# Optimization experiments

Measured on AMD Instinct MI355X. Metric: run time of the kernel, lower is better.

## Reference

```python
import jax, jax.numpy as jnp
import numpy as np

B, C, OUT, H, W, M1, M2, HID = 4, 64, 64, 256, 256, 32, 32, 64
COORD = C + 1  # MLP input: channels + 1 coordinate


def _lin(key, fan_in, fan_out):
    lim = 1.0 / np.sqrt(fan_in)
    kw, kb = jax.random.split(key)
    Wm = jax.random.uniform(kw, (fan_in, fan_out), minval=-lim, maxval=lim, dtype=jnp.float32)
    b = jax.random.uniform(kb, (fan_out,), minval=-lim, maxval=lim, dtype=jnp.float32)
    return Wm, b


def setup_inputs() -> dict:
    key = jax.random.key(0)
    ks = jax.random.split(key, 12)
    x = jax.random.normal(ks[0], (B, C, H, W), dtype=jnp.float32)
    # basis_w MLP: (C+1) -> HID -> HID -> 2*M2
    wW0, wb0 = _lin(ks[1], COORD, HID)
    wW1, wb1 = _lin(ks[2], HID, HID)
    wW2, wb2 = _lin(ks[3], HID, 2 * M2)
    # basis_h MLP: (C+1) -> HID -> HID -> 2*M1
    hW0, hb0 = _lin(ks[4], COORD, HID)
    hW1, hb1 = _lin(ks[5], HID, HID)
    hW2, hb2 = _lin(ks[6], HID, 2 * M1)
    std = (1.0 / (C + OUT)) ** 0.5
    Wf_re = std * jax.random.normal(ks[7], (C, OUT, M1, M2), dtype=jnp.float32)
    Wf_im = std * jax.random.normal(ks[8], (C, OUT, M1, M2), dtype=jnp.float32)
    mixer_w, mixer_b = _lin(ks[9], OUT, OUT)
    mixer_w = mixer_w.T  # (out, in) conv1x1 layout
    sc_w, sc_b = _lin(ks[10], C, OUT)
    sc_w = sc_w.T
    return {
        "x": x,
        "wW0": wW0, "wb0": wb0, "wW1": wW1, "wb1": wb1, "wW2": wW2, "wb2": wb2,
        "hW0": hW0, "hb0": hb0, "hW1": hW1, "hb1": hb1, "hW2": hW2, "hb2": hb2,
        "Wf_re": Wf_re, "Wf_im": Wf_im,
        "mixer_w": mixer_w, "mixer_b": mixer_b,
        "sc_w": sc_w, "sc_b": sc_b,
    }


def _gelu(v):
    return jax.nn.gelu(v, approximate=False)  # torch GELU is exact erf


def _cmlp(x, W0, b0, W1, b1, W2, b2, m):
    h = _gelu(x @ W0 + b0)
    h = _gelu(h @ W1 + b1)
    o = h @ W2 + b2
    return jax.lax.complex(o[..., :m], o[..., m:])


def reference(x, wW0, wb0, wW1, wb1, wW2, wb2,
              hW0, hb0, hW1, hb1, hW2, hb2,
              Wf_re, Wf_im, mixer_w, mixer_b, sc_w, sc_b):
    Bb, Cc, Hh, Ww = x.shape
    # --- W-direction basis: input is (values, w-coord) per pixel ---
    wc = jnp.linspace(-1.0, 1.0, Ww, dtype=jnp.float32)
    w_in = jnp.concatenate(
        [jnp.transpose(x, (0, 2, 3, 1)),
         jnp.broadcast_to(wc[None, None, :, None], (Bb, Hh, Ww, 1))], axis=-1)
    wb = _cmlp(w_in, wW0, wb0, wW1, wb1, wW2, wb2, M2)  # (B,H,W,m2) complex
    xc = x.astype(jnp.complex64)
    # separable transform along W: contract W against runtime basis
    tfw = jnp.einsum('bchw,bhwm->bchm', xc, wb)  # (B,C,H,m2)
    # --- H-direction basis: input is real part of W-transform + h-coord ---
    hcv = jnp.linspace(-1.0, 1.0, Hh, dtype=jnp.float32)
    h_in = jnp.concatenate(
        [jnp.transpose(tfw.real, (0, 3, 2, 1)),
         jnp.broadcast_to(hcv[None, None, :, None], (Bb, M2, Hh, 1))], axis=-1)
    hb = _cmlp(h_in, hW0, hb0, hW1, hb1, hW2, hb2, M1)  # (B,m2,H,m1) complex
    tfhw = jnp.einsum('bchm,bmhk->bckm', tfw, hb)  # (B,C,m1,m2)
    Wf = jax.lax.complex(Wf_re, Wf_im)  # (C_in, C_out, m1, m2)
    proc = jnp.einsum('bixy,oixy->boxy', tfhw, Wf)  # (B,out,m1,m2)
    # inverse transforms with conjugate-transposed bases
    rec = jnp.einsum('bokm,bmhk->bohm', proc, jnp.conj(hb))  # (B,out,H,m2)
    spatial = jnp.einsum('bohm,bhwm->bohw', rec, jnp.conj(wb)).real / (Hh * Ww)
    y = jnp.einsum('bchw,oc->bohw', spatial, mixer_w) + mixer_b[None, :, None, None]
    y = _gelu(y)
    y = y + jnp.einsum('bchw,oc->bohw', x, sc_w) + sc_b[None, :, None, None]
    return _gelu(y)
```

## Files before the change

kernel.cpp:

```cpp
#include <hip/hip_runtime.h>
#include <math.h>


typedef __attribute__((ext_vector_type(8))) short bf16x8;
typedef __attribute__((ext_vector_type(4))) float f32x4;

__device__ __forceinline__ float gelu_f(float v) {
    const float u = v * 0.70710678118654752440f;
    const float xa = fabsf(u);
    const float t = __builtin_amdgcn_rcpf(fmaf(0.3275911f, xa, 1.0f));
    float p = fmaf(1.061405429f, t, -1.453152027f);
    p = fmaf(p, t, 1.421413741f);
    p = fmaf(p, t, -0.284496736f);
    p = fmaf(p, t, 0.254829592f);
    p *= t;
    const float e = __expf(-xa * xa);
    float erfv = fmaf(-p, e, 1.0f);
    erfv = (u < 0.0f) ? -erfv : erfv;
    return 0.5f * v * (1.0f + erfv);
}

__device__ __forceinline__ unsigned short f2b(float f) {
    union { float f; unsigned int u; } v; v.f = f;
    unsigned int u = v.u + 0x7FFFu + ((v.u >> 16) & 1u);
    return (unsigned short)(u >> 16);
}
__device__ __forceinline__ float b2f(unsigned short b) {
    union { unsigned int u; float f; } v; v.u = ((unsigned int)b) << 16;
    return v.f;
}

__device__ __forceinline__ ushort4 butterfly_xT(const float4 v, int q) {
    const float bx = __shfl_xor(v.x, 1);
    const float by = __shfl_xor(v.y, 1);
    const float bz = __shfl_xor(v.z, 1);
    const float bw = __shfl_xor(v.w, 1);
    float4 s1;
    s1.x = ((q & 1) == 0) ? v.x : by;
    s1.y = ((q & 1) == 0) ? bx  : v.y;
    s1.z = ((q & 1) == 0) ? v.z : bw;
    s1.w = ((q & 1) == 0) ? bz  : v.w;
    const float cx = __shfl_xor(s1.x, 2);
    const float cy = __shfl_xor(s1.y, 2);
    const float cz = __shfl_xor(s1.z, 2);
    const float cw = __shfl_xor(s1.w, 2);
    float4 s2;
    s2.x = ((q & 2) == 0) ? s1.x : cz;
    s2.y = ((q & 2) == 0) ? s1.y : cw;
    s2.z = ((q & 2) == 0) ? cx   : s1.z;
    s2.w = ((q & 2) == 0) ? cy   : s1.w;
    ushort4 u;
    u.x = f2b(s2.x); u.y = f2b(s2.y); u.z = f2b(s2.z); u.w = f2b(s2.w);
    return u;
}

__device__ __forceinline__ void stage_xT(const float* __restrict__ x,
    unsigned short* __restrict__ sA, int b, int h, int w0, int t, int LD)
{
    const int lane = t & 63, wv = t >> 6;
    const int q = lane & 3, wg = lane >> 2;
#pragma unroll
    for (int r = 0; r < 4; ++r) {
        const int cb = (r * 4 + wv) * 4;
        const float4 v = *(const float4*)&x[((size_t)(b * 64 + cb + q) * 256 + h) * 256 + w0 + wg * 4];
        const ushort4 u = butterfly_xT(v, q);
        *(ushort4*)&sA[(wg * 4 + q) * LD + cb] = u;
    }
}

__global__ void k_prep(const float* __restrict__ wW0, const float* __restrict__ wW1,
                       const float* __restrict__ wW2,
                       const float* __restrict__ hW0, const float* __restrict__ hW1,
                       const float* __restrict__ hW2,
                       unsigned short* __restrict__ wT0, unsigned short* __restrict__ wT1,
                       unsigned short* __restrict__ wT2,
                       unsigned short* __restrict__ hT0, unsigned short* __restrict__ hT1,
                       unsigned short* __restrict__ hT2)
{
    const int t = threadIdx.x;
    for (int idx = t; idx < 64 * 96; idx += 256) {
        const int o = idx / 96, k = idx % 96;
        wT0[idx] = (k < 65) ? f2b(wW0[k * 64 + o]) : (unsigned short)0;
        hT0[idx] = (k < 65) ? f2b(hW0[k * 64 + o]) : (unsigned short)0;
    }
    for (int idx = t; idx < 4096; idx += 256) {
        const int o = idx >> 6, k = idx & 63;
        wT1[idx] = f2b(wW1[k * 64 + o]);
        wT2[idx] = f2b(wW2[k * 64 + o]);
        hT1[idx] = f2b(hW1[k * 64 + o]);
        hT2[idx] = f2b(hW2[k * 64 + o]);
    }
}

__global__ __launch_bounds__(256) void k_psum(const float* __restrict__ src,
                                              float* __restrict__ dst,
                                              int nparts, int part_stride)
{
    const int i = (blockIdx.x * 256 + threadIdx.x) * 4;
    float4 acc = *(const float4*)&src[i];
    for (int p = 1; p < nparts; ++p) {
        const float4 v = *(const float4*)&src[(size_t)p * part_stride + i];
        acc.x += v.x; acc.y += v.y; acc.z += v.z; acc.w += v.w;
    }
    *(float4*)&dst[i] = acc;
}

__global__ __launch_bounds__(256) void k_psum_procT(const float* __restrict__ src,
                                                    float* __restrict__ dst)
{
    const int idx = blockIdx.x * 256 + threadIdx.x;
    const int o = idx & 63, k = (idx >> 6) & 31, m = (idx >> 11) & 31, b = idx >> 16;
    const size_t in = (size_t)(b * 64 + o) * 1024 + k * 32 + m;
    const float re = src[in] + src[524288 + in];
    const float im = src[262144 + in] + src[524288 + 262144 + in];
    dst[idx] = re;
    dst[262144 + idx] = im;
}

template<bool GELU, int NKC>
__device__ __forceinline__ void mfma_layer_r(
    const bf16x8* __restrict__ wf,
    const unsigned short* __restrict__ sAct,
    unsigned short* __restrict__ dst,
    const float4 bv, int arow, int g, int wv)
{
    const int crow = 16 * wv + g * 4;
    const int sx7 = arow & 7, sx3 = arow & 3;
    const f32x4 zero = {0.f, 0.f, 0.f, 0.f};
    f32x4 acc[4] = {zero, zero, zero, zero};
#pragma unroll
    for (int kc = 0; kc < NKC; ++kc) {
        const int chraw = kc * 4 + g;
        const int ch = (chraw < 8) ? (chraw ^ sx7) : (8 + ((chraw - 8) ^ sx3));
#pragma unroll
        for (int nt = 0; nt < 4; ++nt) {
            const bf16x8 b = *(const bf16x8*)&sAct[(nt * 16 + arow) * 96 + ch * 8];
            acc[nt] = __builtin_amdgcn_mfma_f32_16x16x32_bf16(wf[kc], b, acc[nt], 0, 0, 0);
        }
    }
    const int chw = (crow >> 3) ^ sx7;
#pragma unroll
    for (int nt = 0; nt < 4; ++nt) {
        const int px = nt * 16 + arow;
        float v0 = acc[nt][0] + bv.x;
        float v1 = acc[nt][1] + bv.y;
        float v2 = acc[nt][2] + bv.z;
        float v3 = acc[nt][3] + bv.w;
        if (GELU) { v0 = gelu_f(v0); v1 = gelu_f(v1); v2 = gelu_f(v2); v3 = gelu_f(v3); }
        ushort4 u;
        u.x = f2b(v0); u.y = f2b(v1); u.z = f2b(v2); u.w = f2b(v3);
        *(ushort4*)&dst[px * 96 + chw * 8 + (crow & 7)] = u;
    }
}

__device__ __forceinline__ float4 load_xtile(const float* __restrict__ x,
    int b, int h, int w0, int lane, int wv, int r)
{
    const int q = lane & 3, wg = lane >> 2;
    const int cb = 16 * r + 4 * wv;
    return *(const float4*)&x[((size_t)(b * 64 + cb + q) * 256 + h) * 256 + w0 + wg * 4];
}

__global__ __launch_bounds__(256) void k_wbtfw(
    const float* __restrict__ x,
    const unsigned short* __restrict__ wT0, const float* __restrict__ b0,
    const unsigned short* __restrict__ wT1, const float* __restrict__ b1,
    const unsigned short* __restrict__ wT2, const float* __restrict__ b2,
    unsigned short* __restrict__ wb_bf, unsigned short* __restrict__ tfwM)
{
    __shared__ __align__(16) unsigned short smem[20480];
    unsigned short* sA   = smem;
    unsigned short* sB   = smem + 6144;
    unsigned short* sXt  = smem + 12288;
    unsigned short* sWBt = smem + 16384;

    const int bh = blockIdx.x;
    const int b = bh >> 8, h = bh & 255;
    const int t = threadIdx.x;
    const int lane = t & 63, wv = t >> 6;
    const int arow = lane & 15, g = lane >> 4;
    const int crow = 16 * wv + g * 4;
    const int sx7 = arow & 7;
    const f32x4 zero = {0.f, 0.f, 0.f, 0.f};

    const int wrow = 16 * wv + arow;
    bf16x8 w0f[3], w1f[2], w2f[2];
#pragma unroll
    for (int kc = 0; kc < 3; ++kc)
        w0f[kc] = *(const bf16x8*)&wT0[wrow * 96 + (kc * 4 + g) * 8];
#pragma unroll
    for (int kc = 0; kc < 2; ++kc) {
        w1f[kc] = *(const bf16x8*)&wT1[wrow * 64 + (kc * 4 + g) * 8];
        w2f[kc] = *(const bf16x8*)&wT2[wrow * 64 + (kc * 4 + g) * 8];
    }
    const float4 bv0 = *(const float4*)&b0[crow];
    const float4 bv1 = *(const float4*)&b1[crow];
    const float4 bv2 = *(const float4*)&b2[crow];

    f32x4 atf[4] = {zero, zero, zero, zero};

    float4 xv[4];
#pragma unroll
    for (int r = 0; r < 4; ++r) xv[r] = load_xtile(x, b, h, 0, lane, wv, r);

    for (int wq = 0; wq < 4; ++wq) {
        const int w0 = wq * 64;
        __syncthreads();
        {
            const int q = lane & 3, wg = lane >> 2;
#pragma unroll
            for (int r = 0; r < 4; ++r) {
                const int cb = 16 * r + 4 * wv;
                const int c = cb + q;
                const float4 v = xv[r];
                ushort4 ux;
                ux.x = f2b(v.x); ux.y = f2b(v.y); ux.z = f2b(v.z); ux.w = f2b(v.w);
                const int chx = (wg >> 1) ^ (c & 7);
                *(ushort4*)&sXt[c * 64 + chx * 8 + 4 * (wg & 1)] = ux;
                const ushort4 u = butterfly_xT(v, q);
                const int row = wg * 4 + q;
                const int cha = (cb >> 3) ^ (row & 7);
                *(ushort4*)&sA[row * 96 + cha * 8 + (cb & 7)] = u;
            }
        }
        if (t < 64) {
            const uint4 z = {0, 0, 0, 0};
#pragma unroll
            for (int j = 0; j < 4; ++j)
                *(uint4*)&sA[t * 96 + (8 + (j ^ (t & 3))) * 8] = z;
            sA[t * 96 + (8 + (t & 3)) * 8] = f2b((float)(w0 + t) * (2.0f / 255.0f) - 1.0f);
        }
        float4 xn[4];
        if (wq < 3) {
            const int w0n = (wq + 1) * 64;
#pragma unroll
            for (int r = 0; r < 4; ++r) xn[r] = load_xtile(x, b, h, w0n, lane, wv, r);
        }
        __syncthreads();
        mfma_layer_r<true, 3>(w0f, sA, sB, bv0, arow, g, wv);
        __syncthreads();
        mfma_layer_r<true, 2>(w1f, sB, sA, bv1, arow, g, wv);
        __syncthreads();
        {
            f32x4 acc[4] = {zero, zero, zero, zero};
#pragma unroll
            for (int kc = 0; kc < 2; ++kc) {
                const int ch = (kc * 4 + g) ^ sx7;
#pragma unroll
                for (int nt = 0; nt < 4; ++nt) {
                    const bf16x8 bb = *(const bf16x8*)&sA[(nt * 16 + arow) * 96 + ch * 8];
                    acc[nt] = __builtin_amdgcn_mfma_f32_16x16x32_bf16(w2f[kc], bb, acc[nt], 0, 0, 0);
                }
            }
            const int chw = (crow >> 3) ^ sx7;
#pragma unroll
            for (int nt = 0; nt < 4; ++nt) {
                const int px = nt * 16 + arow;
                ushort4 u;
                u.x = f2b(acc[nt][0] + bv2.x);
                u.y = f2b(acc[nt][1] + bv2.y);
                u.z = f2b(acc[nt][2] + bv2.z);
                u.w = f2b(acc[nt][3] + bv2.w);
                *(ushort4*)&sB[px * 96 + chw * 8 + (crow & 7)] = u;
                const int ph = px >> 3, pl = px & 7;
                sWBt[(crow + 0) * 64 + ((ph ^ ((crow + 0) & 7)) << 3) + pl] = u.x;
                sWBt[(crow + 1) * 64 + ((ph ^ ((crow + 1) & 7)) << 3) + pl] = u.y;
                sWBt[(crow + 2) * 64 + ((ph ^ ((crow + 2) & 7)) << 3) + pl] = u.z;
                sWBt[(crow + 3) * 64 + ((ph ^ ((crow + 3) & 7)) << 3) + pl] = u.w;
            }
        }
        __syncthreads();
        const size_t pixbase = (size_t)(b * 256 + h) * 256 + w0;
#pragma unroll
        for (int r = 0; r < 2; ++r) {
            const int idx = r * 256 + t;
            const int px = idx >> 3, f = idx & 7;
            *(uint4*)&wb_bf[(pixbase + px) * 64 + f * 8] =
                *(const uint4*)&sB[px * 96 + ((f ^ (px & 7)) << 3)];
        }
#pragma unroll
        for (int kc = 0; kc < 2; ++kc) {
            const int ch = (kc * 4 + g) ^ sx7;
            const bf16x8 a = *(const bf16x8*)&sWBt[(16 * wv + arow) * 64 + ch * 8];
#pragma unroll
            for (int nt = 0; nt < 4; ++nt) {
                const bf16x8 bb = *(const bf16x8*)&sXt[(nt * 16 + arow) * 64 + ch * 8];
                atf[nt] = __builtin_amdgcn_mfma_f32_16x16x32_bf16(a, bb, atf[nt], 0, 0, 0);
            }
        }
        if (wq < 3) {
#pragma unroll
            for (int r = 0; r < 4; ++r) xv[r] = xn[r];
        }
    }

    __syncthreads();
    float* sF = (float*)smem;
#pragma unroll
    for (int nt = 0; nt < 4; ++nt) {
        const int c = nt * 16 + arow;
#pragma unroll
        for (int j = 0; j < 4; ++j)
            sF[(crow + j) * 68 + c] = atf[nt][j];
    }
    __syncthreads();
#pragma unroll
    for (int r = 0; r < 4; ++r) {
        const int idx = r * 256 + t;
        const int m = idx >> 5, gg = idx & 31;
        ushort4 u;
        u.x = f2b(sF[m * 68 + gg * 2]);
        u.y = f2b(sF[(m + 32) * 68 + gg * 2]);
        u.z = f2b(sF[m * 68 + gg * 2 + 1]);
        u.w = f2b(sF[(m + 32) * 68 + gg * 2 + 1]);
        *(ushort4*)&tfwM[((size_t)(b * 32 + m) * 256 + h) * 128 + gg * 4] = u;
    }
}

__global__ __launch_bounds__(256) void k_hbtfhw(
    const unsigned short* __restrict__ tfwM,
    const unsigned short* __restrict__ hT0, const float* __restrict__ b0,
    const unsigned short* __restrict__ hT1, const float* __restrict__ b1,
    const unsigned short* __restrict__ hT2, const float* __restrict__ b2,
    unsigned short* __restrict__ hb_bf, float* __restrict__ tfhw_p)
{
    __shared__ __align__(16) unsigned short smem[14336];
    unsigned short* sB = smem;
    unsigned short* sA = smem + 6144;
    float* slab = (float*)(smem + 6144);

    const int blk = blockIdx.x;
    const int bm = blk >> 2, hq = blk & 3;
    const int b = bm >> 5, m = bm & 31;
    const int h0 = hq * 64;
    const int t = threadIdx.x;
    const int lane = t & 63, wv = t >> 6;
    const int arow = lane & 15, g = lane >> 4;
    const int crow = 16 * wv + g * 4;

    const int wrow = 16 * wv + arow;
    bf16x8 h0f[3], h1f[2], h2f[2];
#pragma unroll
    for (int kc = 0; kc < 3; ++kc)
        h0f[kc] = *(const bf16x8*)&hT0[wrow * 96 + (kc * 4 + g) * 8];
#pragma unroll
    for (int kc = 0; kc < 2; ++kc) {
        h1f[kc] = *(const bf16x8*)&hT1[wrow * 64 + (kc * 4 + g) * 8];
        h2f[kc] = *(const bf16x8*)&hT2[wrow * 64 + (kc * 4 + g) * 8];
    }
    const float4 bv0 = *(const float4*)&b0[crow];
    const float4 bv1 = *(const float4*)&b1[crow];
    const float4 bv2 = *(const float4*)&b2[crow];

#pragma unroll
    for (int r = 0; r < 4; ++r) {
        const int idx = r * 256 + t;
        const int p = idx >> 4, f = idx & 15;
        const uint4 raw = *(const uint4*)&tfwM[((size_t)(bm * 256 + h0 + p)) * 128 + f * 8];
        const unsigned short* s = (const unsigned short*)&raw;
        ushort4 u;
        u.x = s[0]; u.y = s[2]; u.z = s[4]; u.w = s[6];
        const int ch = (f >> 1) ^ (p & 7);
        *(ushort4*)&sA[p * 96 + ch * 8 + 4 * (f & 1)] = u;
    }
    if (t < 64) {
        const uint4 z = {0, 0, 0, 0};
#pragma unroll
        for (int j = 0; j < 4; ++j)
            *(uint4*)&sA[t * 96 + (8 + (j ^ (t & 3))) * 8] = z;
        sA[t * 96 + (8 + (t & 3)) * 8] = f2b((float)(h0 + t) * (2.0f / 255.0f) - 1.0f);
    }
    __syncthreads();
    mfma_layer_r<true, 3>(h0f, sA, sB, bv0, arow, g, wv);
    __syncthreads();
    mfma_layer_r<true, 2>(h1f, sB, sA, bv1, arow, g, wv);
    __syncthreads();
    mfma_layer_r<false, 2>(h2f, sA, sB, bv2, arow, g, wv);
    __syncthreads();

    const size_t pixbase = (size_t)bm * 256 + h0;
#pragma unroll
    for (int r = 0; r < 2; ++r) {
        const int idx = r * 256 + t;
        const int px = idx >> 3, f = idx & 7;
        *(uint4*)&hb_bf[(pixbase + px) * 64 + f * 8] =
            *(const uint4*)&sB[px * 96 + ((f ^ (px & 7)) << 3)];
    }

    const int k = t & 31, cq = t >> 5;
    float accr[8], acci[8];
#pragma unroll
    for (int i = 0; i < 8; ++i) { accr[i] = 0.f; acci[i] = 0.f; }
    const size_t tbase = (size_t)bm * 32768;
    for (int ht = 0; ht < 2; ++ht) {
        __syncthreads();
#pragma unroll
        for (int r = 0; r < 2; ++r) {
            const int idx = r * 256 + t;
            const int hl = idx >> 4, f = idx & 15;
            const uint4 raw = *(const uint4*)&tfwM[tbase + (size_t)(h0 + ht * 32 + hl) * 128 + f * 8];
            const unsigned short* s = (const unsigned short*)&raw;
            float4 lo, hi;
            lo.x = b2f(s[0]); lo.y = b2f(s[1]); lo.z = b2f(s[2]); lo.w = b2f(s[3]);
            hi.x = b2f(s[4]); hi.y = b2f(s[5]); hi.z = b2f(s[6]); hi.w = b2f(s[7]);
            *(float4*)&slab[hl * 128 + f * 8] = lo;
            *(float4*)&slab[hl * 128 + f * 8 + 4] = hi;
        }
        __syncthreads();
#pragma unroll 8
        for (int hl = 0; hl < 32; ++hl) {
            const int hrow = ht * 32 + hl;
            const float hrv = b2f(sB[hrow * 96 + (((k >> 3) ^ (hrow & 7)) << 3) + (k & 7)]);
            const float hiv = b2f(sB[hrow * 96 + ((((32 + k) >> 3) ^ (hrow & 7)) << 3) + (k & 7)]);
#pragma unroll
            for (int i2 = 0; i2 < 4; ++i2) {
                const float4 u = *(const float4*)&slab[hl * 128 + cq * 16 + i2 * 4];
                accr[i2 * 2]     = fmaf(u.x, hrv, fmaf(-u.y, hiv, accr[i2 * 2]));
                acci[i2 * 2]     = fmaf(u.x, hiv, fmaf( u.y, hrv, acci[i2 * 2]));
                accr[i2 * 2 + 1] = fmaf(u.z, hrv, fmaf(-u.w, hiv, accr[i2 * 2 + 1]));
                acci[i2 * 2 + 1] = fmaf(u.z, hiv, fmaf( u.w, hrv, acci[i2 * 2 + 1]));
            }
        }
    }
    float* tp = tfhw_p + (size_t)hq * 524288;
#pragma unroll
    for (int i = 0; i < 8; ++i) {
        const int c = cq * 8 + i;
        const size_t po = ((size_t)(b * 64 + c) * 32 + k) * 32 + m;
        tp[po] = accr[i];
        tp[262144 + po] = acci[i];
    }
}

__global__ __launch_bounds__(256) void k_proc2(
    const float* __restrict__ tfhw,
    const float* __restrict__ Wf_re, const float* __restrict__ Wf_im,
    float* __restrict__ proc_p)
{
    const int blk = blockIdx.x;
    const int o = blk >> 3, kq = (blk >> 1) & 3, chalf = blk & 1;
    const int t = threadIdx.x;
    const int mo = kq * 256 + t;
    const float* tre = tfhw;
    const float* tim = tfhw + 262144;
    float accr[4] = {0.f, 0.f, 0.f, 0.f}, acci[4] = {0.f, 0.f, 0.f, 0.f};
    for (int cc = 0; cc < 32; ++cc) {
        const int c = chalf * 32 + cc;
        const float wfr = Wf_re[(size_t)(c * 64 + o) * 1024 + mo];
        const float wfi = Wf_im[(size_t)(c * 64 + o) * 1024 + mo];
#pragma unroll
        for (int bb = 0; bb < 4; ++bb) {
            const float tr = tre[(size_t)(bb * 64 + c) * 1024 + mo];
            const float ti = tim[(size_t)(bb * 64 + c) * 1024 + mo];
            accr[bb] = fmaf(tr, wfr, fmaf(-ti, wfi, accr[bb]));
            acci[bb] = fmaf(tr, wfi, fmaf(ti, wfr, acci[bb]));
        }
    }
    float* pp = proc_p + (size_t)chalf * 524288;
#pragma unroll
    for (int bb = 0; bb < 4; ++bb) {
        pp[(size_t)(bb * 64 + o) * 1024 + mo] = accr[bb];
        pp[262144 + (size_t)(bb * 64 + o) * 1024 + mo] = acci[bb];
    }
}

__global__ __launch_bounds__(256) void k_rec4(
    const float* __restrict__ procT,
    const unsigned short* __restrict__ hb_bf,
    unsigned short* __restrict__ recO)
{
    __shared__ float lhr[32 * 32];
    __shared__ float lhi[32 * 32];
    const int blk = blockIdx.x;
    const int bm = blk >> 3, hq = blk & 7;
    const int b = bm >> 5, m = bm & 31;
    const int t = threadIdx.x;
    {
        const int hl = t >> 3, f = t & 7;
        const uint4 raw = *(const uint4*)&hb_bf[((size_t)bm * 256 + hq * 32 + hl) * 64 + f * 8];
        const unsigned short* us = (const unsigned short*)&raw;
        float v[8];
#pragma unroll
        for (int j = 0; j < 8; ++j) v[j] = b2f(us[j]);
        float* dst = (f < 4) ? &lhr[hl * 32 + f * 8] : &lhi[hl * 32 + (f - 4) * 8];
        float4 lo; lo.x = v[0]; lo.y = v[1]; lo.z = v[2]; lo.w = v[3];
        float4 hi; hi.x = v[4]; hi.y = v[5]; hi.z = v[6]; hi.w = v[7];
        *(float4*)&dst[0] = lo;
        *(float4*)&dst[4] = hi;
    }
    const int o = t & 63, hg = t >> 6;
    const float* pr = procT + (size_t)(b * 32 + m) * 2048 + o;
    const float* pi = pr + 262144;
    float Pr[32], Pi[32];
#pragma unroll
    for (int k = 0; k < 32; ++k) {
        Pr[k] = pr[k * 64];
        Pi[k] = pi[k * 64];
    }
    __syncthreads();
    for (int hh = 0; hh < 8; ++hh) {
        const int hl = hg * 8 + hh;
        float ar = 0.f, ai = 0.f;
#pragma unroll
        for (int k4 = 0; k4 < 8; ++k4) {
            const float4 hr4 = *(const float4*)&lhr[hl * 32 + k4 * 4];
            const float4 hi4 = *(const float4*)&lhi[hl * 32 + k4 * 4];
            ar = fmaf(Pr[k4*4+0], hr4.x, fmaf(Pi[k4*4+0], hi4.x, ar));
            ai = fmaf(Pi[k4*4+0], hr4.x, fmaf(-Pr[k4*4+0], hi4.x, ai));
            ar = fmaf(Pr[k4*4+1], hr4.y, fmaf(Pi[k4*4+1], hi4.y, ar));
            ai = fmaf(Pi[k4*4+1], hr4.y, fmaf(-Pr[k4*4+1], hi4.y, ai));
            ar = fmaf(Pr[k4*4+2], hr4.z, fmaf(Pi[k4*4+2], hi4.z, ar));
            ai = fmaf(Pi[k4*4+2], hr4.z, fmaf(-Pr[k4*4+2], hi4.z, ai));
            ar = fmaf(Pr[k4*4+3], hr4.w, fmaf(Pi[k4*4+3], hi4.w, ar));
            ai = fmaf(Pi[k4*4+3], hr4.w, fmaf(-Pr[k4*4+3], hi4.w, ai));
        }
        const int h = hq * 32 + hl;
        const size_t rb = ((size_t)(b * 256 + h) * 64 + o) * 64;
        recO[rb + m]      = f2b(ar);
        recO[rb + 32 + m] = f2b(ai);
    }
}

__global__ __launch_bounds__(256) void k_final4(
    const float* __restrict__ x,
    const unsigned short* __restrict__ wb_bf,
    const unsigned short* __restrict__ recO,
    const float* __restrict__ mw, const float* __restrict__ mb,
    const float* __restrict__ scw, const float* __restrict__ scb,
    float* __restrict__ out)
{
    constexpr int LD = 72;
    __shared__ __align__(16) unsigned short sWb[64 * LD];
    __shared__ __align__(16) unsigned short sR [64 * LD];
    __shared__ __align__(16) unsigned short sX [64 * LD];
    __shared__ __align__(16) unsigned short sS [64 * LD];
    const int blk = blockIdx.x;
    const int b = blk >> 10, h = (blk >> 2) & 255, wq = blk & 3;
    const int w0 = wq * 64;
    const int t = threadIdx.x;
    const int lane = t & 63, wv = t >> 6;
    const size_t pixbase = (size_t)(b * 256 + h) * 256 + w0;

    float4 mwv[4], scv[4];
#pragma unroll
    for (int r = 0; r < 4; ++r) {
        const int idx = r * 256 + t;
        const int o = idx >> 4, cq2 = idx & 15;
        mwv[r] = *(const float4*)&mw[o * 64 + cq2 * 4];
        scv[r] = *(const float4*)&scw[o * 64 + cq2 * 4];
    }

#pragma unroll
    for (int r = 0; r < 2; ++r) {
        const int idx = r * 256 + t;
        const int px = idx >> 3, f = idx & 7;
        *(uint4*)&sWb[px * LD + f * 8] = *(const uint4*)&wb_bf[(pixbase + px) * 64 + f * 8];
    }
    const size_t recbase = (size_t)(b * 256 + h) * 4096;
#pragma unroll
    for (int r = 0; r < 2; ++r) {
        const int idx = r * 256 + t;
        const int o = idx >> 3, f = idx & 7;
        *(uint4*)&sR[o * LD + f * 8] = *(const uint4*)&recO[recbase + (size_t)o * 64 + f * 8];
    }
    stage_xT(x, sX, b, h, w0, t, LD);
    __syncthreads();

    const int arow = lane & 15;
    const int koff = (lane >> 4) * 8;
    const f32x4 zero = {0.f, 0.f, 0.f, 0.f};

    f32x4 accA[4] = {zero, zero, zero, zero};
#pragma unroll
    for (int kc = 0; kc < 2; ++kc) {
        const bf16x8 a = *(const bf16x8*)&sR[(16 * wv + arow) * LD + kc * 32 + koff];
#pragma unroll
        for (int nt = 0; nt < 4; ++nt) {
            const bf16x8 bb = *(const bf16x8*)&sWb[(nt * 16 + arow) * LD + kc * 32 + koff];
            accA[nt] = __builtin_amdgcn_mfma_f32_16x16x32_bf16(a, bb, accA[nt], 0, 0, 0);
        }
    }
    __syncthreads();

    const int crow = 16 * wv + (lane >> 4) * 4;
#pragma unroll
    for (int nt = 0; nt < 4; ++nt) {
        const int px = nt * 16 + arow;
#pragma unroll
        for (int j = 0; j < 4; ++j)
            sS[px * LD + crow + j] = f2b(accA[nt][j] * (1.0f / 65536.0f));
    }
#pragma unroll
    for (int r = 0; r < 4; ++r) {
        const int idx = r * 256 + t;
        const int o = idx >> 4, cq2 = idx & 15;
        ushort4 u1;
        u1.x = f2b(mwv[r].x); u1.y = f2b(mwv[r].y); u1.z = f2b(mwv[r].z); u1.w = f2b(mwv[r].w);
        *(ushort4*)&sWb[o * LD + cq2 * 4] = u1;
        ushort4 u2;
        u2.x = f2b(scv[r].x); u2.y = f2b(scv[r].y); u2.z = f2b(scv[r].z); u2.w = f2b(scv[r].w);
        *(ushort4*)&sR[o * LD + cq2 * 4] = u2;
    }
    __syncthreads();

    f32x4 accB[4] = {zero, zero, zero, zero};
    f32x4 accC[4] = {zero, zero, zero, zero};
#pragma unroll
    for (int kc = 0; kc < 2; ++kc) {
        const bf16x8 am = *(const bf16x8*)&sWb[(16 * wv + arow) * LD + kc * 32 + koff];
        const bf16x8 as = *(const bf16x8*)&sR [(16 * wv + arow) * LD + kc * 32 + koff];
#pragma unroll
        for (int nt = 0; nt < 4; ++nt) {
            const bf16x8 bs = *(const bf16x8*)&sS[(nt * 16 + arow) * LD + kc * 32 + koff];
            const bf16x8 bx = *(const bf16x8*)&sX[(nt * 16 + arow) * LD + kc * 32 + koff];
            accB[nt] = __builtin_amdgcn_mfma_f32_16x16x32_bf16(am, bs, accB[nt], 0, 0, 0);
            accC[nt] = __builtin_amdgcn_mfma_f32_16x16x32_bf16(as, bx, accC[nt], 0, 0, 0);
        }
    }

#pragma unroll
    for (int nt = 0; nt < 4; ++nt) {
        const int px = nt * 16 + arow;
#pragma unroll
        for (int j = 0; j < 4; ++j) {
            const int o = crow + j;
            const float y = gelu_f(accB[nt][j] + mb[o]);
            const float z = y + accC[nt][j] + scb[o];
            out[((size_t)(b * 64 + o) * 256 + h) * 256 + w0 + px] = gelu_f(z);
        }
    }
}

extern "C" void kernel_launch(void* const* d_in, const int* in_sizes, int n_in,
                              void* d_out, int out_size, void* d_ws, size_t ws_size,
                              hipStream_t stream) {
    const float* x    = (const float*)d_in[0];
    const float* wW0  = (const float*)d_in[1];
    const float* wb0  = (const float*)d_in[2];
    const float* wW1  = (const float*)d_in[3];
    const float* wb1  = (const float*)d_in[4];
    const float* wW2  = (const float*)d_in[5];
    const float* wb2  = (const float*)d_in[6];
    const float* hW0  = (const float*)d_in[7];
    const float* hb0  = (const float*)d_in[8];
    const float* hW1  = (const float*)d_in[9];
    const float* hb1  = (const float*)d_in[10];
    const float* hW2  = (const float*)d_in[11];
    const float* hb2  = (const float*)d_in[12];
    const float* Wf_re = (const float*)d_in[13];
    const float* Wf_im = (const float*)d_in[14];
    const float* mw   = (const float*)d_in[15];
    const float* mbv  = (const float*)d_in[16];
    const float* scw  = (const float*)d_in[17];
    const float* scb  = (const float*)d_in[18];

    char* base = (char*)d_ws;
    unsigned short* wb_bf = (unsigned short*)(base + 0);
    unsigned short* tfwM  = (unsigned short*)(base + 33554432);
    unsigned short* hb_bf = (unsigned short*)(base + 41943040);
    float* tfhw_p = (float*)(base + 46137344);
    float* tfhw   = (float*)(base + 54525952);
    float* proc_p = (float*)(base + 56623104);
    float* procT  = (float*)(base + 60817408);
    unsigned short* recO = (unsigned short*)(base + 62914560);
    unsigned short* wT0 = (unsigned short*)(base + 71303168);
    unsigned short* wT1 = (unsigned short*)(base + 71315456);
    unsigned short* wT2 = (unsigned short*)(base + 71323648);
    unsigned short* hT0 = (unsigned short*)(base + 71331840);
    unsigned short* hT1 = (unsigned short*)(base + 71344128);
    unsigned short* hT2 = (unsigned short*)(base + 71352320);

    k_prep<<<1, 256, 0, stream>>>(wW0, wW1, wW2, hW0, hW1, hW2,
                                  wT0, wT1, wT2, hT0, hT1, hT2);
    k_wbtfw<<<1024, 256, 0, stream>>>(x, wT0, wb0, wT1, wb1, wT2, wb2,
                                      wb_bf, tfwM);
    k_hbtfhw<<<512, 256, 0, stream>>>(tfwM, hT0, hb0, hT1, hb1, hT2, hb2,
                                      hb_bf, tfhw_p);
    k_psum<<<1024, 256, 0, stream>>>(tfhw_p, tfhw, 4, 524288);
    k_proc2<<<512, 256, 0, stream>>>(tfhw, Wf_re, Wf_im, proc_p);
    k_psum_procT<<<1024, 256, 0, stream>>>(proc_p, procT);
    k_rec4<<<1024, 256, 0, stream>>>(procT, hb_bf, recO);
    k_final4<<<4096, 256, 0, stream>>>(x, wb_bf, recO, mw, mbv, scw, scb,
                                       (float*)d_out);
}
```

Baseline: 177.3 us.

## Fuse middle pipeline stages into one cooperative kernel with grid syncs

Merges the H-basis/tfhw, partial-sum reduction, spectral weight multiply, proc transpose-reduce and inverse H reconstruction kernels into one cooperative kernel of 512 blocks, separated by grid-wide syncs. This removes four kernel launches and their launch gaps, at the cost of grid barriers and a fixed 512-block grid, so the reduction and reconstruction stages do twice the work per block. It also vectorizes one shared-memory store in the final kernel into a single ushort4 write.

```diff
diff --git a/kernel.cpp b/kernel.cpp
--- a/kernel.cpp
+++ b/kernel.cpp
@@ -1,5 +1,8 @@
 #include <hip/hip_runtime.h>
+#include <hip/hip_cooperative_groups.h>
 #include <math.h>
+
+namespace cg = cooperative_groups;
 
 
 typedef __attribute__((ext_vector_type(8))) short bf16x8;
@@ -92,31 +95,6 @@
     }
 }
 
-__global__ __launch_bounds__(256) void k_psum(const float* __restrict__ src,
-                                              float* __restrict__ dst,
-                                              int nparts, int part_stride)
-{
-    const int i = (blockIdx.x * 256 + threadIdx.x) * 4;
-    float4 acc = *(const float4*)&src[i];
-    for (int p = 1; p < nparts; ++p) {
-        const float4 v = *(const float4*)&src[(size_t)p * part_stride + i];
-        acc.x += v.x; acc.y += v.y; acc.z += v.z; acc.w += v.w;
-    }
-    *(float4*)&dst[i] = acc;
-}
-
-__global__ __launch_bounds__(256) void k_psum_procT(const float* __restrict__ src,
-                                                    float* __restrict__ dst)
-{
-    const int idx = blockIdx.x * 256 + threadIdx.x;
-    const int o = idx & 63, k = (idx >> 6) & 31, m = (idx >> 11) & 31, b = idx >> 16;
-    const size_t in = (size_t)(b * 64 + o) * 1024 + k * 32 + m;
-    const float re = src[in] + src[524288 + in];
-    const float im = src[262144 + in] + src[524288 + 262144 + in];
-    dst[idx] = re;
-    dst[262144 + idx] = im;
-}
-
 template<bool GELU, int NKC>
 __device__ __forceinline__ void mfma_layer_r(
     const bf16x8* __restrict__ wf,
@@ -317,207 +295,235 @@
     }
 }
 
-__global__ __launch_bounds__(256) void k_hbtfhw(
+__global__ __launch_bounds__(256) void k_mid(
     const unsigned short* __restrict__ tfwM,
     const unsigned short* __restrict__ hT0, const float* __restrict__ b0,
     const unsigned short* __restrict__ hT1, const float* __restrict__ b1,
     const unsigned short* __restrict__ hT2, const float* __restrict__ b2,
-    unsigned short* __restrict__ hb_bf, float* __restrict__ tfhw_p)
+    unsigned short* __restrict__ hb_bf, float* __restrict__ tfhw_p,
+    float* __restrict__ tfhw,
+    const float* __restrict__ Wf_re, const float* __restrict__ Wf_im,
+    float* __restrict__ proc_p, float* __restrict__ procT,
+    unsigned short* __restrict__ recO)
 {
+    cg::grid_group gridg = cg::this_grid();
     __shared__ __align__(16) unsigned short smem[14336];
-    unsigned short* sB = smem;
-    unsigned short* sA = smem + 6144;
-    float* slab = (float*)(smem + 6144);
-
     const int blk = blockIdx.x;
-    const int bm = blk >> 2, hq = blk & 3;
-    const int b = bm >> 5, m = bm & 31;
-    const int h0 = hq * 64;
     const int t = threadIdx.x;
     const int lane = t & 63, wv = t >> 6;
-    const int arow = lane & 15, g = lane >> 4;
-    const int crow = 16 * wv + g * 4;
-
-    const int wrow = 16 * wv + arow;
-    bf16x8 h0f[3], h1f[2], h2f[2];
-#pragma unroll
-    for (int kc = 0; kc < 3; ++kc)
-        h0f[kc] = *(const bf16x8*)&hT0[wrow * 96 + (kc * 4 + g) * 8];
-#pragma unroll
-    for (int kc = 0; kc < 2; ++kc) {
-        h1f[kc] = *(const bf16x8*)&hT1[wrow * 64 + (kc * 4 + g) * 8];
-        h2f[kc] = *(const bf16x8*)&hT2[wrow * 64 + (kc * 4 + g) * 8];
-    }
-    const float4 bv0 = *(const float4*)&b0[crow];
-    const float4 bv1 = *(const float4*)&b1[crow];
-    const float4 bv2 = *(const float4*)&b2[crow];
-
-#pragma unroll
-    for (int r = 0; r < 4; ++r) {
-        const int idx = r * 256 + t;
-        const int p = idx >> 4, f = idx & 15;
-        const uint4 raw = *(const uint4*)&tfwM[((size_t)(bm * 256 + h0 + p)) * 128 + f * 8];
-        const unsigned short* s = (const unsigned short*)&raw;
-        ushort4 u;
-        u.x = s[0]; u.y = s[2]; u.z = s[4]; u.w = s[6];
-        const int ch = (f >> 1) ^ (p & 7);
-        *(ushort4*)&sA[p * 96 + ch * 8 + 4 * (f & 1)] = u;
-    }
-    if (t < 64) {
-        const uint4 z = {0, 0, 0, 0};
-#pragma unroll
-        for (int j = 0; j < 4; ++j)
-            *(uint4*)&sA[t * 96 + (8 + (j ^ (t & 3))) * 8] = z;
-        sA[t * 96 + (8 + (t & 3)) * 8] = f2b((float)(h0 + t) * (2.0f / 255.0f) - 1.0f);
-    }
-    __syncthreads();
-    mfma_layer_r<true, 3>(h0f, sA, sB, bv0, arow, g, wv);
-    __syncthreads();
-    mfma_layer_r<true, 2>(h1f, sB, sA, bv1, arow, g, wv);
-    __syncthreads();
-    mfma_layer_r<false, 2>(h2f, sA, sB, bv2, arow, g, wv);
-    __syncthreads();
-
-    const size_t pixbase = (size_t)bm * 256 + h0;
-#pragma unroll
-    for (int r = 0; r < 2; ++r) {
-        const int idx = r * 256 + t;
-        const int px = idx >> 3, f = idx & 7;
-        *(uint4*)&hb_bf[(pixbase + px) * 64 + f * 8] =
-            *(const uint4*)&sB[px * 96 + ((f ^ (px & 7)) << 3)];
-    }
-
-    const int k = t & 31, cq = t >> 5;
-    float accr[8], acci[8];
-#pragma unroll
-    for (int i = 0; i < 8; ++i) { accr[i] = 0.f; acci[i] = 0.f; }
-    const size_t tbase = (size_t)bm * 32768;
-    for (int ht = 0; ht < 2; ++ht) {
-        __syncthreads();
+
+    {
+        unsigned short* sB = smem;
+        unsigned short* sA = smem + 6144;
+        float* slab = (float*)(smem + 6144);
+
+        const int bm = blk >> 2, hq = blk & 3;
+        const int b = bm >> 5, m = bm & 31;
+        const int h0 = hq * 64;
+        const int arow = lane & 15, g = lane >> 4;
+        const int crow = 16 * wv + g * 4;
+
+        const int wrow = 16 * wv + arow;
+        bf16x8 h0f[3], h1f[2], h2f[2];
+#pragma unroll
+        for (int kc = 0; kc < 3; ++kc)
+            h0f[kc] = *(const bf16x8*)&hT0[wrow * 96 + (kc * 4 + g) * 8];
+#pragma unroll
+        for (int kc = 0; kc < 2; ++kc) {
+            h1f[kc] = *(const bf16x8*)&hT1[wrow * 64 + (kc * 4 + g) * 8];
+            h2f[kc] = *(const bf16x8*)&hT2[wrow * 64 + (kc * 4 + g) * 8];
+        }
+        const float4 bv0 = *(const float4*)&b0[crow];
+        const float4 bv1 = *(const float4*)&b1[crow];
+        const float4 bv2 = *(const float4*)&b2[crow];
+
+#pragma unroll
+        for (int r = 0; r < 4; ++r) {
+            const int idx = r * 256 + t;
+            const int p = idx >> 4, f = idx & 15;
+            const uint4 raw = *(const uint4*)&tfwM[((size_t)(bm * 256 + h0 + p)) * 128 + f * 8];
+            const unsigned short* s = (const unsigned short*)&raw;
+            ushort4 u;
+            u.x = s[0]; u.y = s[2]; u.z = s[4]; u.w = s[6];
+            const int ch = (f >> 1) ^ (p & 7);
+            *(ushort4*)&sA[p * 96 + ch * 8 + 4 * (f & 1)] = u;
+        }
+        if (t < 64) {
+            const uint4 z = {0, 0, 0, 0};
+#pragma unroll
+            for (int j = 0; j < 4; ++j)
+                *(uint4*)&sA[t * 96 + (8 + (j ^ (t & 3))) * 8] = z;
+            sA[t * 96 + (8 + (t & 3)) * 8] = f2b((float)(h0 + t) * (2.0f / 255.0f) - 1.0f);
+        }
+        __syncthreads();
+        mfma_layer_r<true, 3>(h0f, sA, sB, bv0, arow, g, wv);
+        __syncthreads();
+        mfma_layer_r<true, 2>(h1f, sB, sA, bv1, arow, g, wv);
+        __syncthreads();
+        mfma_layer_r<false, 2>(h2f, sA, sB, bv2, arow, g, wv);
+        __syncthreads();
+
+        const size_t pixbase = (size_t)bm * 256 + h0;
 #pragma unroll
         for (int r = 0; r < 2; ++r) {
             const int idx = r * 256 + t;
-            const int hl = idx >> 4, f = idx & 15;
-            const uint4 raw = *(const uint4*)&tfwM[tbase + (size_t)(h0 + ht * 32 + hl) * 128 + f * 8];
-            const unsigned short* s = (const unsigned short*)&raw;
-            float4 lo, hi;
-            lo.x = b2f(s[0]); lo.y = b2f(s[1]); lo.z = b2f(s[2]); lo.w = b2f(s[3]);
-            hi.x = b2f(s[4]); hi.y = b2f(s[5]); hi.z = b2f(s[6]); hi.w = b2f(s[7]);
-            *(float4*)&slab[hl * 128 + f * 8] = lo;
-            *(float4*)&slab[hl * 128 + f * 8 + 4] = hi;
-        }
-        __syncthreads();
+            const int px = idx >> 3, f = idx & 7;
+            *(uint4*)&hb_bf[(pixbase + px) * 64 + f * 8] =
+                *(const uint4*)&sB[px * 96 + ((f ^ (px & 7)) << 3)];
+        }
+
+        const int k = t & 31, cq = t >> 5;
+        float accr[8], acci[8];
+#pragma unroll
+        for (int i = 0; i < 8; ++i) { accr[i] = 0.f; acci[i] = 0.f; }
+        const size_t tbase = (size_t)bm * 32768;
+        for (int ht = 0; ht < 2; ++ht) {
+            __syncthreads();
+#pragma unroll
+            for (int r = 0; r < 2; ++r) {
+                const int idx = r * 256 + t;
+                const int hl = idx >> 4, f = idx & 15;
+                const uint4 raw = *(const uint4*)&tfwM[tbase + (size_t)(h0 + ht * 32 + hl) * 128 + f * 8];
+                const unsigned short* s = (const unsigned short*)&raw;
+                float4 lo, hi;
+                lo.x = b2f(s[0]); lo.y = b2f(s[1]); lo.z = b2f(s[2]); lo.w = b2f(s[3]);
+                hi.x = b2f(s[4]); hi.y = b2f(s[5]); hi.z = b2f(s[6]); hi.w = b2f(s[7]);
+                *(float4*)&slab[hl * 128 + f * 8] = lo;
+                *(float4*)&slab[hl * 128 + f * 8 + 4] = hi;
+            }
+            __syncthreads();
 #pragma unroll 8
-        for (int hl = 0; hl < 32; ++hl) {
-            const int hrow = ht * 32 + hl;
-            const float hrv = b2f(sB[hrow * 96 + (((k >> 3) ^ (hrow & 7)) << 3) + (k & 7)]);
-            const float hiv = b2f(sB[hrow * 96 + ((((32 + k) >> 3) ^ (hrow & 7)) << 3) + (k & 7)]);
-#pragma unroll
-            for (int i2 = 0; i2 < 4; ++i2) {
-                const float4 u = *(const float4*)&slab[hl * 128 + cq * 16 + i2 * 4];
-                accr[i2 * 2]     = fmaf(u.x, hrv, fmaf(-u.y, hiv, accr[i2 * 2]));
-                acci[i2 * 2]     = fmaf(u.x, hiv, fmaf( u.y, hrv, acci[i2 * 2]));
-                accr[i2 * 2 + 1] = fmaf(u.z, hrv, fmaf(-u.w, hiv, accr[i2 * 2 + 1]));
-                acci[i2 * 2 + 1] = fmaf(u.z, hiv, fmaf( u.w, hrv, acci[i2 * 2 + 1]));
-            }
-        }
-    }
-    float* tp = tfhw_p + (size_t)hq * 524288;
-#pragma unroll
-    for (int i = 0; i < 8; ++i) {
-        const int c = cq * 8 + i;
-        const size_t po = ((size_t)(b * 64 + c) * 32 + k) * 32 + m;
-        tp[po] = accr[i];
-        tp[262144 + po] = acci[i];
-    }
-}
-
-__global__ __launch_bounds__(256) void k_proc2(
-    const float* __restrict__ tfhw,
-    const float* __restrict__ Wf_re, const float* __restrict__ Wf_im,
-    float* __restrict__ proc_p)
-{
-    const int blk = blockIdx.x;
-    const int o = blk >> 3, kq = (blk >> 1) & 3, chalf = blk & 1;
-    const int t = threadIdx.x;
-    const int mo = kq * 256 + t;
-    const float* tre = tfhw;
-    const float* tim = tfhw + 262144;
-    float accr[4] = {0.f, 0.f, 0.f, 0.f}, acci[4] = {0.f, 0.f, 0.f, 0.f};
-    for (int cc = 0; cc < 32; ++cc) {
-        const int c = chalf * 32 + cc;
-        const float wfr = Wf_re[(size_t)(c * 64 + o) * 1024 + mo];
-        const float wfi = Wf_im[(size_t)(c * 64 + o) * 1024 + mo];
+            for (int hl = 0; hl < 32; ++hl) {
+                const int hrow = ht * 32 + hl;
+                const float hrv = b2f(sB[hrow * 96 + (((k >> 3) ^ (hrow & 7)) << 3) + (k & 7)]);
+                const float hiv = b2f(sB[hrow * 96 + ((((32 + k) >> 3) ^ (hrow & 7)) << 3) + (k & 7)]);
+#pragma unroll
+                for (int i2 = 0; i2 < 4; ++i2) {
+                    const float4 u = *(const float4*)&slab[hl * 128 + cq * 16 + i2 * 4];
+                    accr[i2 * 2]     = fmaf(u.x, hrv, fmaf(-u.y, hiv, accr[i2 * 2]));
+                    acci[i2 * 2]     = fmaf(u.x, hiv, fmaf( u.y, hrv, acci[i2 * 2]));
+                    accr[i2 * 2 + 1] = fmaf(u.z, hrv, fmaf(-u.w, hiv, accr[i2 * 2 + 1]));
+                    acci[i2 * 2 + 1] = fmaf(u.z, hiv, fmaf( u.w, hrv, acci[i2 * 2 + 1]));
+                }
+            }
+        }
+        float* tp = tfhw_p + (size_t)hq * 524288;
+#pragma unroll
+        for (int i = 0; i < 8; ++i) {
+            const int c = cq * 8 + i;
+            const size_t po = ((size_t)(b * 64 + c) * 32 + k) * 32 + m;
+            tp[po] = accr[i];
+            tp[262144 + po] = acci[i];
+        }
+    }
+    gridg.sync();
+
+    {
+        const int i = (blk * 256 + t) * 4;
+        float4 acc = *(const float4*)&tfhw_p[i];
+#pragma unroll
+        for (int p = 1; p < 4; ++p) {
+            const float4 v = *(const float4*)&tfhw_p[(size_t)p * 524288 + i];
+            acc.x += v.x; acc.y += v.y; acc.z += v.z; acc.w += v.w;
+        }
+        *(float4*)&tfhw[i] = acc;
+    }
+    gridg.sync();
+
+    {
+        const int o = blk >> 3, kq = (blk >> 1) & 3, chalf = blk & 1;
+        const int mo = kq * 256 + t;
+        const float* tre = tfhw;
+        const float* tim = tfhw + 262144;
+        float accr[4] = {0.f, 0.f, 0.f, 0.f}, acci[4] = {0.f, 0.f, 0.f, 0.f};
+        for (int cc = 0; cc < 32; ++cc) {
+            const int c = chalf * 32 + cc;
+            const float wfr = Wf_re[(size_t)(c * 64 + o) * 1024 + mo];
+            const float wfi = Wf_im[(size_t)(c * 64 + o) * 1024 + mo];
+#pragma unroll
+            for (int bb = 0; bb < 4; ++bb) {
+                const float tr = tre[(size_t)(bb * 64 + c) * 1024 + mo];
+                const float ti = tim[(size_t)(bb * 64 + c) * 1024 + mo];
+                accr[bb] = fmaf(tr, wfr, fmaf(-ti, wfi, accr[bb]));
+                acci[bb] = fmaf(tr, wfi, fmaf(ti, wfr, acci[bb]));
+            }
+        }
+        float* pp = proc_p + (size_t)chalf * 524288;
 #pragma unroll
         for (int bb = 0; bb < 4; ++bb) {
-            const float tr = tre[(size_t)(bb * 64 + c) * 1024 + mo];
-            const float ti = tim[(size_t)(bb * 64 + c) * 1024 + mo];
-            accr[bb] = fmaf(tr, wfr, fmaf(-ti, wfi, accr[bb]));
-            acci[bb] = fmaf(tr, wfi, fmaf(ti, wfr, acci[bb]));
-        }
-    }
-    float* pp = proc_p + (size_t)chalf * 524288;
-#pragma unroll
-    for (int bb = 0; bb < 4; ++bb) {
-        pp[(size_t)(bb * 64 + o) * 1024 + mo] = accr[bb];
-        pp[262144 + (size_t)(bb * 64 + o) * 1024 + mo] = acci[bb];
-    }
-}
-
-__global__ __launch_bounds__(256) void k_rec4(
-    const float* __restrict__ procT,
-    const unsigned short* __restrict__ hb_bf,
-    unsigned short* __restrict__ recO)
-{
-    __shared__ float lhr[32 * 32];
-    __shared__ float lhi[32 * 32];
-    const int blk = blockIdx.x;
-    const int bm = blk >> 3, hq = blk & 7;
-    const int b = bm >> 5, m = bm & 31;
-    const int t = threadIdx.x;
+            pp[(size_t)(bb * 64 + o) * 1024 + mo] = accr[bb];
+            pp[262144 + (size_t)(bb * 64 + o) * 1024 + mo] = acci[bb];
+        }
+    }
+    gridg.sync();
+
     {
-        const int hl = t >> 3, f = t & 7;
-        const uint4 raw = *(const uint4*)&hb_bf[((size_t)bm * 256 + hq * 32 + hl) * 64 + f * 8];
-        const unsigned short* us = (const unsigned short*)&raw;
-        float v[8];
-#pragma unroll
-        for (int j = 0; j < 8; ++j) v[j] = b2f(us[j]);
-        float* dst = (f < 4) ? &lhr[hl * 32 + f * 8] : &lhi[hl * 32 + (f - 4) * 8];
-        float4 lo; lo.x = v[0]; lo.y = v[1]; lo.z = v[2]; lo.w = v[3];
-        float4 hi; hi.x = v[4]; hi.y = v[5]; hi.z = v[6]; hi.w = v[7];
-        *(float4*)&dst[0] = lo;
-        *(float4*)&dst[4] = hi;
-    }
-    const int o = t & 63, hg = t >> 6;
-    const float* pr = procT + (size_t)(b * 32 + m) * 2048 + o;
-    const float* pi = pr + 262144;
-    float Pr[32], Pi[32];
-#pragma unroll
-    for (int k = 0; k < 32; ++k) {
-        Pr[k] = pr[k * 64];
-        Pi[k] = pi[k * 64];
-    }
-    __syncthreads();
-    for (int hh = 0; hh < 8; ++hh) {
-        const int hl = hg * 8 + hh;
-        float ar = 0.f, ai = 0.f;
-#pragma unroll
-        for (int k4 = 0; k4 < 8; ++k4) {
-            const float4 hr4 = *(const float4*)&lhr[hl * 32 + k4 * 4];
-            const float4 hi4 = *(const float4*)&lhi[hl * 32 + k4 * 4];
-            ar = fmaf(Pr[k4*4+0], hr4.x, fmaf(Pi[k4*4+0], hi4.x, ar));
-            ai = fmaf(Pi[k4*4+0], hr4.x, fmaf(-Pr[k4*4+0], hi4.x, ai));
-            ar = fmaf(Pr[k4*4+1], hr4.y, fmaf(Pi[k4*4+1], hi4.y, ar));
-            ai = fmaf(Pi[k4*4+1], hr4.y, fmaf(-Pr[k4*4+1], hi4.y, ai));
-            ar = fmaf(Pr[k4*4+2], hr4.z, fmaf(Pi[k4*4+2], hi4.z, ar));
-            ai = fmaf(Pi[k4*4+2], hr4.z, fmaf(-Pr[k4*4+2], hi4.z, ai));
-            ar = fmaf(Pr[k4*4+3], hr4.w, fmaf(Pi[k4*4+3], hi4.w, ar));
-            ai = fmaf(Pi[k4*4+3], hr4.w, fmaf(-Pr[k4*4+3], hi4.w, ai));
-        }
-        const int h = hq * 32 + hl;
-        const size_t rb = ((size_t)(b * 256 + h) * 64 + o) * 64;
-        recO[rb + m]      = f2b(ar);
-        recO[rb + 32 + m] = f2b(ai);
+#pragma unroll
+        for (int r = 0; r < 2; ++r) {
+            const int idx = r * 131072 + blk * 256 + t;
+            const int o = idx & 63, k = (idx >> 6) & 31, m = (idx >> 11) & 31, b = idx >> 16;
+            const size_t in = (size_t)(b * 64 + o) * 1024 + k * 32 + m;
+            const float re = proc_p[in] + proc_p[524288 + in];
+            const float im = proc_p[262144 + in] + proc_p[524288 + 262144 + in];
+            procT[idx] = re;
+            procT[262144 + idx] = im;
+        }
+    }
+    gridg.sync();
+
+    {
+        float* lhr = (float*)smem;
+        float* lhi = lhr + 1024;
+        const int bm = blk >> 2;
+        const int b = bm >> 5, m = bm & 31;
+        const int o = t & 63, hg = t >> 6;
+        const float* pr = procT + (size_t)(b * 32 + m) * 2048 + o;
+        const float* pi = pr + 262144;
+        float Pr[32], Pi[32];
+#pragma unroll
+        for (int k = 0; k < 32; ++k) {
+            Pr[k] = pr[k * 64];
+            Pi[k] = pi[k * 64];
+        }
+        for (int it = 0; it < 2; ++it) {
+            const int hq = (blk & 3) * 2 + it;
+            __syncthreads();
+            {
+                const int hl = t >> 3, f = t & 7;
+                const uint4 raw = *(const uint4*)&hb_bf[((size_t)bm * 256 + hq * 32 + hl) * 64 + f * 8];
+                const unsigned short* us = (const unsigned short*)&raw;
+                float v[8];
+#pragma unroll
+                for (int j = 0; j < 8; ++j) v[j] = b2f(us[j]);
+                float* dst = (f < 4) ? &lhr[hl * 32 + f * 8] : &lhi[hl * 32 + (f - 4) * 8];
+                float4 lo; lo.x = v[0]; lo.y = v[1]; lo.z = v[2]; lo.w = v[3];
+                float4 hi; hi.x = v[4]; hi.y = v[5]; hi.z = v[6]; hi.w = v[7];
+                *(float4*)&dst[0] = lo;
+                *(float4*)&dst[4] = hi;
+            }
+            __syncthreads();
+            for (int hh = 0; hh < 8; ++hh) {
+                const int hl = hg * 8 + hh;
+                float ar = 0.f, ai = 0.f;
+#pragma unroll
+                for (int k4 = 0; k4 < 8; ++k4) {
+                    const float4 hr4 = *(const float4*)&lhr[hl * 32 + k4 * 4];
+                    const float4 hi4 = *(const float4*)&lhi[hl * 32 + k4 * 4];
+                    ar = fmaf(Pr[k4*4+0], hr4.x, fmaf(Pi[k4*4+0], hi4.x, ar));
+                    ai = fmaf(Pi[k4*4+0], hr4.x, fmaf(-Pr[k4*4+0], hi4.x, ai));
+                    ar = fmaf(Pr[k4*4+1], hr4.y, fmaf(Pi[k4*4+1], hi4.y, ar));
+                    ai = fmaf(Pi[k4*4+1], hr4.y, fmaf(-Pr[k4*4+1], hi4.y, ai));
+                    ar = fmaf(Pr[k4*4+2], hr4.z, fmaf(Pi[k4*4+2], hi4.z, ar));
+                    ai = fmaf(Pi[k4*4+2], hr4.z, fmaf(-Pr[k4*4+2], hi4.z, ai));
+                    ar = fmaf(Pr[k4*4+3], hr4.w, fmaf(Pi[k4*4+3], hi4.w, ar));
+                    ai = fmaf(Pi[k4*4+3], hr4.w, fmaf(-Pr[k4*4+3], hi4.w, ai));
+                }
+                const int h = hq * 32 + hl;
+                const size_t rb = ((size_t)(b * 256 + h) * 64 + o) * 64;
+                recO[rb + m]      = f2b(ar);
+                recO[rb + 32 + m] = f2b(ai);
+            }
+        }
     }
 }
 
@@ -586,9 +592,12 @@
 #pragma unroll
     for (int nt = 0; nt < 4; ++nt) {
         const int px = nt * 16 + arow;
-#pragma unroll
-        for (int j = 0; j < 4; ++j)
-            sS[px * LD + crow + j] = f2b(accA[nt][j] * (1.0f / 65536.0f));
+        ushort4 u;
+        u.x = f2b(accA[nt][0] * (1.0f / 65536.0f));
+        u.y = f2b(accA[nt][1] * (1.0f / 65536.0f));
+        u.z = f2b(accA[nt][2] * (1.0f / 65536.0f));
+        u.w = f2b(accA[nt][3] * (1.0f / 65536.0f));
+        *(ushort4*)&sS[px * LD + crow] = u;
     }
 #pragma unroll
     for (int r = 0; r < 4; ++r) {
@@ -674,12 +683,31 @@
                                   wT0, wT1, wT2, hT0, hT1, hT2);
     k_wbtfw<<<1024, 256, 0, stream>>>(x, wT0, wb0, wT1, wb1, wT2, wb2,
                                       wb_bf, tfwM);
-    k_hbtfhw<<<512, 256, 0, stream>>>(tfwM, hT0, hb0, hT1, hb1, hT2, hb2,
-                                      hb_bf, tfhw_p);
-    k_psum<<<1024, 256, 0, stream>>>(tfhw_p, tfhw, 4, 524288);
-    k_proc2<<<512, 256, 0, stream>>>(tfhw, Wf_re, Wf_im, proc_p);
-    k_psum_procT<<<1024, 256, 0, stream>>>(proc_p, procT);
-    k_rec4<<<1024, 256, 0, stream>>>(procT, hb_bf, recO);
+    {
+        const unsigned short* a_tfwM = tfwM;
+        const unsigned short* a_hT0 = hT0; const float* a_b0 = hb0;
+        const unsigned short* a_hT1 = hT1; const float* a_b1 = hb1;
+        const unsigned short* a_hT2 = hT2; const float* a_b2 = hb2;
+        unsigned short* a_hb = hb_bf;
+        float* a_tfhw_p = tfhw_p;
+        float* a_tfhw = tfhw;
+        const float* a_wfr = Wf_re;
+        const float* a_wfi = Wf_im;
+        float* a_proc_p = proc_p;
+        float* a_procT = procT;
+        unsigned short* a_recO = recO;
+        void* args[] = {
+            (void*)&a_tfwM,
+            (void*)&a_hT0, (void*)&a_b0,
+            (void*)&a_hT1, (void*)&a_b1,
+            (void*)&a_hT2, (void*)&a_b2,
+            (void*)&a_hb, (void*)&a_tfhw_p, (void*)&a_tfhw,
+            (void*)&a_wfr, (void*)&a_wfi,
+            (void*)&a_proc_p, (void*)&a_procT, (void*)&a_recO
+        };
+        hipLaunchCooperativeKernel((void*)k_mid, dim3(512), dim3(256),
+                                   args, 0, stream);
+    }
     k_final4<<<4096, 256, 0, stream>>>(x, wb_bf, recO, mw, mbv, scw, scb,
                                        (float*)d_out);
 }
```

Result: slower. 424.2 us (+139.2%).
